# Performance work log

Measured on AMD Instinct MI355X. Metric: run time of the kernel, lower is better.

The kernel has to match this reference:

```python
import jax, jax.numpy as jnp
import numpy as np

B, C, H, W = 4, 64, 64, 64
CQK = C // 8


def setup_inputs() -> dict:
    key = jax.random.key(0)
    k0, k1, k2, k3, k4 = jax.random.split(key, 5)
    x = jax.random.normal(k0, (B, C, H, W), dtype=jnp.float32)
    # Conv1d kernel_size=1, bias=False -> plain [out, in] matmul weights
    Wq = jax.random.normal(k1, (CQK, C), dtype=jnp.float32) * 0.05
    Wk = jax.random.normal(k2, (CQK, C), dtype=jnp.float32) * 0.05
    Wv = jax.random.normal(k3, (C, C), dtype=jnp.float32) * 0.05
    # torch init is 0; use a nonzero scalar so the attention path is exercised
    gamma = jax.random.uniform(k4, (1,), dtype=jnp.float32)
    return {"x": x, "Wq": Wq, "Wk": Wk, "Wv": Wv, "gamma": gamma}


def reference(x, Wq, Wk, Wv, gamma):
    shape = x.shape                      # [B, C, H, W]
    xf = x.reshape(shape[0], shape[1], -1)  # [B, C, N]
    q = jnp.einsum('oc,bcn->bon', Wq, xf)   # [B, C/8, N]
    k = jnp.einsum('oc,bcn->bon', Wk, xf)   # [B, C/8, N]
    v = jnp.einsum('oc,bcn->bon', Wv, xf)   # [B, C, N]
    # score[b, n, m] = sum_c q[b, c, n] * k[b, c, m]  (no 1/sqrt(d) scale)
    score = jnp.einsum('bcn,bcm->bnm', q, k)  # [B, N, N]
    # unconventional softmax over dim=1 (rows/first N axis, i.e. per-column)
    score = jax.nn.softmax(score, axis=1)
    out = jnp.einsum('bcn,bnm->bcm', v, score)  # [B, C, N]
    attention = gamma * out + xf
    return attention.reshape(shape)
```

## Files before the change

kernel.cpp:

```cpp
#include <hip/hip_runtime.h>

#define BB 4
#define NN 4096

typedef __attribute__((ext_vector_type(8))) short short8v;
typedef __attribute__((ext_vector_type(4))) short short4v;
typedef __attribute__((ext_vector_type(4))) float float4v;

__device__ __forceinline__ unsigned short f2bf_rn(float f) {
    unsigned u = __float_as_uint(f);
    u += 0x7FFFu + ((u >> 16) & 1u);
    return (unsigned short)(u >> 16);
}

__global__ __launch_bounds__(256) void qkv_kernel(
    const float* __restrict__ x,
    const float* __restrict__ Wq, const float* __restrict__ Wk,
    const float* __restrict__ Wv,
    unsigned short* __restrict__ Qt, unsigned short* __restrict__ Kt,
    unsigned short* __restrict__ Vsw)
{
    __shared__ float xs[64][68];
    __shared__ float wl[64][81];
    __shared__ unsigned short Ot[80][72];

    const int t  = threadIdx.x;
    const int b  = blockIdx.y;
    const int n0 = blockIdx.x * 64;

    #pragma unroll
    for (int i = 0; i < 20; ++i) {
        int idx = t + 256 * i;
        int r = idx >> 6, c = idx & 63;
        float w;
        if (r < 8)       w = Wq[r * 64 + c];
        else if (r < 16) w = Wk[(r - 8) * 64 + c];
        else             w = Wv[(r - 16) * 64 + c];
        wl[c][r] = w;
    }
    #pragma unroll
    for (int i = 0; i < 4; ++i) {
        int idx = t + 256 * i;
        int c = idx >> 4, n4 = (idx & 15) * 4;
        *(float4*)&xs[c][n4] = *(const float4*)&x[(size_t)(b * 64 + c) * NN + n0 + n4];
    }
    __syncthreads();

    const int n4 = (t & 15) * 4;
    const int og = t >> 4;

    float acc[5][4];
    #pragma unroll
    for (int k = 0; k < 5; ++k)
        #pragma unroll
        for (int i = 0; i < 4; ++i) acc[k][i] = 0.f;

    for (int c = 0; c < 64; ++c) {
        float4 xv = *(const float4*)&xs[c][n4];
        #pragma unroll
        for (int k = 0; k < 5; ++k) {
            float wv = wl[c][og * 5 + k];
            acc[k][0] += wv * xv.x;
            acc[k][1] += wv * xv.y;
            acc[k][2] += wv * xv.z;
            acc[k][3] += wv * xv.w;
        }
    }

    #pragma unroll
    for (int k = 0; k < 5; ++k) {
        short4v pk;
        #pragma unroll
        for (int i = 0; i < 4; ++i) pk[i] = (short)f2bf_rn(acc[k][i]);
        *(short4v*)&Ot[og * 5 + k][n4] = pk;
    }
    __syncthreads();

    if (t < 128) {
        int n = t & 63;
        int rbase = (t < 64) ? 0 : 8;
        short8v p;
        #pragma unroll
        for (int j = 0; j < 8; ++j) p[j] = (short)Ot[rbase + j][n];
        unsigned short* dst = ((t < 64) ? Qt : Kt) + ((size_t)b * NN + n0 + n) * 8;
        *(short8v*)dst = p;
    }

    {
        int ci = t >> 5, s = t & 31;
        int ct = ci >> 1, nbl = ci & 1;
        size_t nb = (size_t)blockIdx.x * 2 + nbl;
        unsigned short* cb = Vsw + ((size_t)(b * 4 + ct) * 128 + nb) * 512;
        #pragma unroll
        for (int h = 0; h < 2; ++h) {
            int l = s * 2 + h;
            short8v d = *(short8v*)&Ot[16 + ct * 16 + (l & 15)][nbl * 32 + ((l >> 4) << 3)];
            *(short8v*)(cb + l * 8) = d;
        }
    }
}

__global__ __launch_bounds__(256, 4) void attn_kernel(
    const unsigned short* __restrict__ Qt,
    const unsigned short* __restrict__ Kt,
    const unsigned short* __restrict__ Vsw,
    const float* __restrict__ x, const float* __restrict__ gamma,
    float* __restrict__ out)
{
    __shared__ __align__(16) unsigned short Pb[4][2][16][40];
    __shared__ float Ored[4][64][17];
    __shared__ float Lred[4][16];
    __shared__ float Lf[16];

    const int t    = threadIdx.x;
    const int w    = t >> 6;
    const int lane = t & 63;
    const int quad = lane >> 4;
    const int l15  = lane & 15;
    const int b    = blockIdx.y;
    const int m0   = blockIdx.x * 16;

    const short8v zfrag = {0, 0, 0, 0, 0, 0, 0, 0};
    const float4v zacc  = {0.f, 0.f, 0.f, 0.f};

    short8v bk = zfrag;
    if (quad == 0)
        bk = *(const short8v*)(Kt + (size_t)(b * NN + m0 + l15) * 8);

    float4v acc[4];
    #pragma unroll
    for (int ct = 0; ct < 4; ++ct) acc[ct] = zacc;
    float Lacc = 0.f;

    const unsigned short* qrow = Qt + (size_t)(b * NN + w * 1024 + l15) * 8;
    const unsigned short* vptr = Vsw + ((size_t)b * 4 * 128 + w * 32) * 512 + lane * 8;

    short8v av0 = *(const short8v*)(vptr);
    short8v av1 = *(const short8v*)(vptr + 1 * 128 * 512);
    short8v av2 = *(const short8v*)(vptr + 2 * 128 * 512);
    short8v av3 = *(const short8v*)(vptr + 3 * 128 * 512);
    {
        short8v aq0 = zfrag, aq1 = zfrag;
        if (quad == 0) {
            aq0 = *(const short8v*)(qrow);
            aq1 = *(const short8v*)(qrow + 16 * 8);
        }
        float4v s0 = __builtin_amdgcn_mfma_f32_16x16x32_bf16(aq0, bk, zacc, 0, 0, 0);
        float4v s1 = __builtin_amdgcn_mfma_f32_16x16x32_bf16(aq1, bk, zacc, 0, 0, 0);
        float p[8];
        #pragma unroll
        for (int j = 0; j < 4; ++j) p[j]     = __expf(s0[j]);
        #pragma unroll
        for (int j = 0; j < 4; ++j) p[4 + j] = __expf(s1[j]);
        #pragma unroll
        for (int j = 0; j < 8; ++j) Lacc += p[j];
        short4v pk0, pk1;
        #pragma unroll
        for (int j = 0; j < 4; ++j) {
            pk0[j] = (short)f2bf_rn(p[j]);
            pk1[j] = (short)f2bf_rn(p[4 + j]);
        }
        *(short4v*)&Pb[w][0][l15][quad * 4]      = pk0;
        *(short4v*)&Pb[w][0][l15][16 + quad * 4] = pk1;
    }

    for (int it = 0; it < 31; ++it) {
        const int itn = it + 1;

        short8v avn0 = *(const short8v*)(vptr + itn * 512);
        short8v avn1 = *(const short8v*)(vptr + 1 * 128 * 512 + itn * 512);
        short8v avn2 = *(const short8v*)(vptr + 2 * 128 * 512 + itn * 512);
        short8v avn3 = *(const short8v*)(vptr + 3 * 128 * 512 + itn * 512);

        short8v aq0 = zfrag, aq1 = zfrag;
        if (quad == 0) {
            aq0 = *(const short8v*)(qrow + (size_t)(itn * 32) * 8);
            aq1 = *(const short8v*)(qrow + (size_t)(itn * 32 + 16) * 8);
        }
        float4v s0 = __builtin_amdgcn_mfma_f32_16x16x32_bf16(aq0, bk, zacc, 0, 0, 0);
        float4v s1 = __builtin_amdgcn_mfma_f32_16x16x32_bf16(aq1, bk, zacc, 0, 0, 0);
        float p[8];
        #pragma unroll
        for (int j = 0; j < 4; ++j) p[j]     = __expf(s0[j]);
        #pragma unroll
        for (int j = 0; j < 4; ++j) p[4 + j] = __expf(s1[j]);
        #pragma unroll
        for (int j = 0; j < 8; ++j) Lacc += p[j];
        short4v pk0, pk1;
        #pragma unroll
        for (int j = 0; j < 4; ++j) {
            pk0[j] = (short)f2bf_rn(p[j]);
            pk1[j] = (short)f2bf_rn(p[4 + j]);
        }
        *(short4v*)&Pb[w][itn & 1][l15][quad * 4]      = pk0;
        *(short4v*)&Pb[w][itn & 1][l15][16 + quad * 4] = pk1;

        short8v bp = *(const short8v*)&Pb[w][it & 1][l15][quad * 8];
        acc[0] = __builtin_amdgcn_mfma_f32_16x16x32_bf16(av0, bp, acc[0], 0, 0, 0);
        acc[1] = __builtin_amdgcn_mfma_f32_16x16x32_bf16(av1, bp, acc[1], 0, 0, 0);
        acc[2] = __builtin_amdgcn_mfma_f32_16x16x32_bf16(av2, bp, acc[2], 0, 0, 0);
        acc[3] = __builtin_amdgcn_mfma_f32_16x16x32_bf16(av3, bp, acc[3], 0, 0, 0);

        av0 = avn0; av1 = avn1; av2 = avn2; av3 = avn3;
    }

    {
        short8v bp = *(const short8v*)&Pb[w][1][l15][quad * 8];
        acc[0] = __builtin_amdgcn_mfma_f32_16x16x32_bf16(av0, bp, acc[0], 0, 0, 0);
        acc[1] = __builtin_amdgcn_mfma_f32_16x16x32_bf16(av1, bp, acc[1], 0, 0, 0);
        acc[2] = __builtin_amdgcn_mfma_f32_16x16x32_bf16(av2, bp, acc[2], 0, 0, 0);
        acc[3] = __builtin_amdgcn_mfma_f32_16x16x32_bf16(av3, bp, acc[3], 0, 0, 0);
    }

    Lacc += __shfl_xor(Lacc, 16, 64);
    Lacc += __shfl_xor(Lacc, 32, 64);
    if (lane < 16) Lred[w][lane] = Lacc;

    #pragma unroll
    for (int ct = 0; ct < 4; ++ct)
        #pragma unroll
        for (int r = 0; r < 4; ++r)
            Ored[w][ct * 16 + quad * 4 + r][l15] = acc[ct][r];
    __syncthreads();

    if (t < 16)
        Lf[t] = 1.f / (Lred[0][t] + Lred[1][t] + Lred[2][t] + Lred[3][t]);
    __syncthreads();

    {
        const float gv = gamma[0];
        int c = t >> 2, m4 = (t & 3) * 4;
        float4 o;
        #pragma unroll
        for (int i = 0; i < 4; ++i) {
            float s = Ored[0][c][m4 + i] + Ored[1][c][m4 + i]
                    + Ored[2][c][m4 + i] + Ored[3][c][m4 + i];
            ((float*)&o)[i] = s * Lf[m4 + i];
        }
        size_t gbase = (size_t)(b * 64 + c) * NN + m0 + m4;
        float4 xv = *(const float4*)&x[gbase];
        float4 r;
        r.x = gv * o.x + xv.x; r.y = gv * o.y + xv.y;
        r.z = gv * o.z + xv.z; r.w = gv * o.w + xv.w;
        *(float4*)&out[gbase] = r;
    }
}

extern "C" void kernel_launch(void* const* d_in, const int* in_sizes, int n_in,
                              void* d_out, int out_size, void* d_ws, size_t ws_size,
                              hipStream_t stream) {
    const float* x     = (const float*)d_in[0];
    const float* Wq    = (const float*)d_in[1];
    const float* Wk    = (const float*)d_in[2];
    const float* Wv    = (const float*)d_in[3];
    const float* gamma = (const float*)d_in[4];
    float* out = (float*)d_out;

    unsigned short* ws = (unsigned short*)d_ws;
    unsigned short* Qt  = ws;
    unsigned short* Kt  = Qt + (size_t)BB * NN * 8;
    unsigned short* Vsw = Kt + (size_t)BB * NN * 8;

    qkv_kernel<<<dim3(NN / 64, BB), 256, 0, stream>>>(x, Wq, Wk, Wv, Qt, Kt, Vsw);
    attn_kernel<<<dim3(NN / 16, BB), 256, 0, stream>>>(Qt, Kt, Vsw, x, gamma, out);
}
```

Measured before the change: 97.10 us.

## Deepen attention prefetch, union LDS buffers, halve QKV tile, pack bf16 via perm

The attention loop now prefetches Q and V fragments two iterations ahead and issues the P-buffer read and score MFMAs before the exp work, aiming to hide global load latency. The P buffer and output reduction buffer share LDS through a union, which cuts shared memory per block and may raise occupancy; this needs an extra barrier before reuse. The QKV kernel processes 32 columns per block instead of 64, doubling the grid for better CU coverage at the cost of more redundant weight loads. The bf16 pairs are packed with a byte-permute intrinsic, which should need fewer instructions.

```diff
diff --git a/kernel.cpp b/kernel.cpp
--- a/kernel.cpp
+++ b/kernel.cpp
@@ -11,6 +11,13 @@
     unsigned u = __float_as_uint(f);
     u += 0x7FFFu + ((u >> 16) & 1u);
     return (unsigned short)(u >> 16);
+}
+
+__device__ __forceinline__ unsigned pack2_rte(float fa, float fb) {
+    unsigned a = __float_as_uint(fa), b = __float_as_uint(fb);
+    a = a + 0x7FFFu + ((a >> 16) & 1u);
+    b = b + 0x7FFFu + ((b >> 16) & 1u);
+    return __builtin_amdgcn_perm(b, a, 0x07060302u);
 }
 
 __global__ __launch_bounds__(256) void qkv_kernel(
@@ -20,13 +27,14 @@
     unsigned short* __restrict__ Qt, unsigned short* __restrict__ Kt,
     unsigned short* __restrict__ Vsw)
 {
-    __shared__ float xs[64][68];
+    __shared__ float xs[64][36];
     __shared__ float wl[64][81];
-    __shared__ unsigned short Ot[80][72];
+    __shared__ unsigned short Ot[80][40];
 
     const int t  = threadIdx.x;
     const int b  = blockIdx.y;
-    const int n0 = blockIdx.x * 64;
+    const int nb = blockIdx.x;
+    const int n0 = nb * 32;
 
     #pragma unroll
     for (int i = 0; i < 20; ++i) {
@@ -39,66 +47,59 @@
         wl[c][r] = w;
     }
     #pragma unroll
-    for (int i = 0; i < 4; ++i) {
+    for (int i = 0; i < 2; ++i) {
         int idx = t + 256 * i;
-        int c = idx >> 4, n4 = (idx & 15) * 4;
+        int c = idx >> 3, n4 = (idx & 7) * 4;
         *(float4*)&xs[c][n4] = *(const float4*)&x[(size_t)(b * 64 + c) * NN + n0 + n4];
     }
     __syncthreads();
 
-    const int n4 = (t & 15) * 4;
+    const int n2 = (t & 15) * 2;
     const int og = t >> 4;
 
-    float acc[5][4];
-    #pragma unroll
-    for (int k = 0; k < 5; ++k)
-        #pragma unroll
-        for (int i = 0; i < 4; ++i) acc[k][i] = 0.f;
+    float acc[5][2];
+    #pragma unroll
+    for (int k = 0; k < 5; ++k) { acc[k][0] = 0.f; acc[k][1] = 0.f; }
 
     for (int c = 0; c < 64; ++c) {
-        float4 xv = *(const float4*)&xs[c][n4];
+        float2 xv = *(const float2*)&xs[c][n2];
         #pragma unroll
         for (int k = 0; k < 5; ++k) {
             float wv = wl[c][og * 5 + k];
             acc[k][0] += wv * xv.x;
             acc[k][1] += wv * xv.y;
-            acc[k][2] += wv * xv.z;
-            acc[k][3] += wv * xv.w;
         }
     }
 
     #pragma unroll
     for (int k = 0; k < 5; ++k) {
-        short4v pk;
-        #pragma unroll
-        for (int i = 0; i < 4; ++i) pk[i] = (short)f2bf_rn(acc[k][i]);
-        *(short4v*)&Ot[og * 5 + k][n4] = pk;
-    }
-    __syncthreads();
-
-    if (t < 128) {
-        int n = t & 63;
-        int rbase = (t < 64) ? 0 : 8;
+        Ot[og * 5 + k][n2]     = f2bf_rn(acc[k][0]);
+        Ot[og * 5 + k][n2 + 1] = f2bf_rn(acc[k][1]);
+    }
+    __syncthreads();
+
+    if (t < 64) {
+        int n = t & 31;
+        int rbase = (t < 32) ? 0 : 8;
         short8v p;
         #pragma unroll
         for (int j = 0; j < 8; ++j) p[j] = (short)Ot[rbase + j][n];
-        unsigned short* dst = ((t < 64) ? Qt : Kt) + ((size_t)b * NN + n0 + n) * 8;
+        unsigned short* dst = ((t < 32) ? Qt : Kt) + ((size_t)b * NN + n0 + n) * 8;
         *(short8v*)dst = p;
     }
 
     {
-        int ci = t >> 5, s = t & 31;
-        int ct = ci >> 1, nbl = ci & 1;
-        size_t nb = (size_t)blockIdx.x * 2 + nbl;
+        int ct = t >> 6, l = t & 63;
         unsigned short* cb = Vsw + ((size_t)(b * 4 + ct) * 128 + nb) * 512;
-        #pragma unroll
-        for (int h = 0; h < 2; ++h) {
-            int l = s * 2 + h;
-            short8v d = *(short8v*)&Ot[16 + ct * 16 + (l & 15)][nbl * 32 + ((l >> 4) << 3)];
-            *(short8v*)(cb + l * 8) = d;
-        }
-    }
-}
+        short8v d = *(short8v*)&Ot[16 + ct * 16 + (l & 15)][(l >> 4) * 8];
+        *(short8v*)(cb + l * 8) = d;
+    }
+}
+
+union AttnSmem {
+    unsigned short Pb[4][2][16][40];
+    float Ored[4][64][17];
+};
 
 __global__ __launch_bounds__(256, 4) void attn_kernel(
     const unsigned short* __restrict__ Qt,
@@ -107,8 +108,7 @@
     const float* __restrict__ x, const float* __restrict__ gamma,
     float* __restrict__ out)
 {
-    __shared__ __align__(16) unsigned short Pb[4][2][16][40];
-    __shared__ float Ored[4][64][17];
+    __shared__ __align__(16) AttnSmem sm;
     __shared__ float Lred[4][16];
     __shared__ float Lf[16];
 
@@ -149,63 +149,65 @@
         float4v s1 = __builtin_amdgcn_mfma_f32_16x16x32_bf16(aq1, bk, zacc, 0, 0, 0);
         float p[8];
         #pragma unroll
-        for (int j = 0; j < 4; ++j) p[j]     = __expf(s0[j]);
-        #pragma unroll
-        for (int j = 0; j < 4; ++j) p[4 + j] = __expf(s1[j]);
+        for (int j = 0; j < 4; ++j) { p[j] = __expf(s0[j]); p[4 + j] = __expf(s1[j]); }
         #pragma unroll
         for (int j = 0; j < 8; ++j) Lacc += p[j];
-        short4v pk0, pk1;
-        #pragma unroll
-        for (int j = 0; j < 4; ++j) {
-            pk0[j] = (short)f2bf_rn(p[j]);
-            pk1[j] = (short)f2bf_rn(p[4 + j]);
-        }
-        *(short4v*)&Pb[w][0][l15][quad * 4]      = pk0;
-        *(short4v*)&Pb[w][0][l15][16 + quad * 4] = pk1;
+        unsigned pk0 = pack2_rte(p[0], p[1]), pk1 = pack2_rte(p[2], p[3]);
+        unsigned pk2 = pack2_rte(p[4], p[5]), pk3 = pack2_rte(p[6], p[7]);
+        *(uint2*)&sm.Pb[w][0][l15][quad * 4]      = make_uint2(pk0, pk1);
+        *(uint2*)&sm.Pb[w][0][l15][16 + quad * 4] = make_uint2(pk2, pk3);
+    }
+    short8v avn0 = *(const short8v*)(vptr + 512);
+    short8v avn1 = *(const short8v*)(vptr + 1 * 128 * 512 + 512);
+    short8v avn2 = *(const short8v*)(vptr + 2 * 128 * 512 + 512);
+    short8v avn3 = *(const short8v*)(vptr + 3 * 128 * 512 + 512);
+    short8v aqn0 = zfrag, aqn1 = zfrag;
+    if (quad == 0) {
+        aqn0 = *(const short8v*)(qrow + 32 * 8);
+        aqn1 = *(const short8v*)(qrow + 48 * 8);
     }
 
     for (int it = 0; it < 31; ++it) {
         const int itn = it + 1;
-
-        short8v avn0 = *(const short8v*)(vptr + itn * 512);
-        short8v avn1 = *(const short8v*)(vptr + 1 * 128 * 512 + itn * 512);
-        short8v avn2 = *(const short8v*)(vptr + 2 * 128 * 512 + itn * 512);
-        short8v avn3 = *(const short8v*)(vptr + 3 * 128 * 512 + itn * 512);
-
-        short8v aq0 = zfrag, aq1 = zfrag;
+        const int i2  = (it + 2) & 31;
+
+        short8v bp = *(const short8v*)&sm.Pb[w][it & 1][l15][quad * 8];
+
+        float4v s0 = __builtin_amdgcn_mfma_f32_16x16x32_bf16(aqn0, bk, zacc, 0, 0, 0);
+        float4v s1 = __builtin_amdgcn_mfma_f32_16x16x32_bf16(aqn1, bk, zacc, 0, 0, 0);
+
+        short8v a2q0 = zfrag, a2q1 = zfrag;
         if (quad == 0) {
-            aq0 = *(const short8v*)(qrow + (size_t)(itn * 32) * 8);
-            aq1 = *(const short8v*)(qrow + (size_t)(itn * 32 + 16) * 8);
-        }
-        float4v s0 = __builtin_amdgcn_mfma_f32_16x16x32_bf16(aq0, bk, zacc, 0, 0, 0);
-        float4v s1 = __builtin_amdgcn_mfma_f32_16x16x32_bf16(aq1, bk, zacc, 0, 0, 0);
+            a2q0 = *(const short8v*)(qrow + (size_t)(i2 * 32) * 8);
+            a2q1 = *(const short8v*)(qrow + (size_t)(i2 * 32 + 16) * 8);
+        }
+        short8v a2v0 = *(const short8v*)(vptr + i2 * 512);
+        short8v a2v1 = *(const short8v*)(vptr + 1 * 128 * 512 + i2 * 512);
+        short8v a2v2 = *(const short8v*)(vptr + 2 * 128 * 512 + i2 * 512);
+        short8v a2v3 = *(const short8v*)(vptr + 3 * 128 * 512 + i2 * 512);
+
         float p[8];
         #pragma unroll
-        for (int j = 0; j < 4; ++j) p[j]     = __expf(s0[j]);
-        #pragma unroll
-        for (int j = 0; j < 4; ++j) p[4 + j] = __expf(s1[j]);
+        for (int j = 0; j < 4; ++j) { p[j] = __expf(s0[j]); p[4 + j] = __expf(s1[j]); }
         #pragma unroll
         for (int j = 0; j < 8; ++j) Lacc += p[j];
-        short4v pk0, pk1;
-        #pragma unroll
-        for (int j = 0; j < 4; ++j) {
-            pk0[j] = (short)f2bf_rn(p[j]);
-            pk1[j] = (short)f2bf_rn(p[4 + j]);
-        }
-        *(short4v*)&Pb[w][itn & 1][l15][quad * 4]      = pk0;
-        *(short4v*)&Pb[w][itn & 1][l15][16 + quad * 4] = pk1;
-
-        short8v bp = *(const short8v*)&Pb[w][it & 1][l15][quad * 8];
+        unsigned pk0 = pack2_rte(p[0], p[1]), pk1 = pack2_rte(p[2], p[3]);
+        unsigned pk2 = pack2_rte(p[4], p[5]), pk3 = pack2_rte(p[6], p[7]);
+        *(uint2*)&sm.Pb[w][itn & 1][l15][quad * 4]      = make_uint2(pk0, pk1);
+        *(uint2*)&sm.Pb[w][itn & 1][l15][16 + quad * 4] = make_uint2(pk2, pk3);
+
         acc[0] = __builtin_amdgcn_mfma_f32_16x16x32_bf16(av0, bp, acc[0], 0, 0, 0);
         acc[1] = __builtin_amdgcn_mfma_f32_16x16x32_bf16(av1, bp, acc[1], 0, 0, 0);
         acc[2] = __builtin_amdgcn_mfma_f32_16x16x32_bf16(av2, bp, acc[2], 0, 0, 0);
         acc[3] = __builtin_amdgcn_mfma_f32_16x16x32_bf16(av3, bp, acc[3], 0, 0, 0);
 
         av0 = avn0; av1 = avn1; av2 = avn2; av3 = avn3;
-    }
-
-    {
-        short8v bp = *(const short8v*)&Pb[w][1][l15][quad * 8];
+        avn0 = a2v0; avn1 = a2v1; avn2 = a2v2; avn3 = a2v3;
+        aqn0 = a2q0; aqn1 = a2q1;
+    }
+
+    {
+        short8v bp = *(const short8v*)&sm.Pb[w][1][l15][quad * 8];
         acc[0] = __builtin_amdgcn_mfma_f32_16x16x32_bf16(av0, bp, acc[0], 0, 0, 0);
         acc[1] = __builtin_amdgcn_mfma_f32_16x16x32_bf16(av1, bp, acc[1], 0, 0, 0);
         acc[2] = __builtin_amdgcn_mfma_f32_16x16x32_bf16(av2, bp, acc[2], 0, 0, 0);
@@ -216,13 +218,13 @@
     Lacc += __shfl_xor(Lacc, 32, 64);
     if (lane < 16) Lred[w][lane] = Lacc;
 
+    __syncthreads();
+
     #pragma unroll
     for (int ct = 0; ct < 4; ++ct)
         #pragma unroll
         for (int r = 0; r < 4; ++r)
-            Ored[w][ct * 16 + quad * 4 + r][l15] = acc[ct][r];
-    __syncthreads();
-
+            sm.Ored[w][ct * 16 + quad * 4 + r][l15] = acc[ct][r];
     if (t < 16)
         Lf[t] = 1.f / (Lred[0][t] + Lred[1][t] + Lred[2][t] + Lred[3][t]);
     __syncthreads();
@@ -233,8 +235,8 @@
         float4 o;
         #pragma unroll
         for (int i = 0; i < 4; ++i) {
-            float s = Ored[0][c][m4 + i] + Ored[1][c][m4 + i]
-                    + Ored[2][c][m4 + i] + Ored[3][c][m4 + i];
+            float s = sm.Ored[0][c][m4 + i] + sm.Ored[1][c][m4 + i]
+                    + sm.Ored[2][c][m4 + i] + sm.Ored[3][c][m4 + i];
             ((float*)&o)[i] = s * Lf[m4 + i];
         }
         size_t gbase = (size_t)(b * 64 + c) * NN + m0 + m4;
@@ -261,6 +263,6 @@
     unsigned short* Kt  = Qt + (size_t)BB * NN * 8;
     unsigned short* Vsw = Kt + (size_t)BB * NN * 8;
 
-    qkv_kernel<<<dim3(NN / 64, BB), 256, 0, stream>>>(x, Wq, Wk, Wv, Qt, Kt, Vsw);
+    qkv_kernel<<<dim3(NN / 32, BB), 256, 0, stream>>>(x, Wq, Wk, Wv, Qt, Kt, Vsw);
     attn_kernel<<<dim3(NN / 16, BB), 256, 0, stream>>>(Qt, Kt, Vsw, x, gamma, out);
 }
```

Result: no change. 97.76 us (+0.7%).
